# Kernel tuning notes

Measured on AMD Instinct MI355X. Metric: run time of the kernel, lower is better.

The kernel has to match this reference:

```python
import jax, jax.numpy as jnp
import numpy as np

jax.config.update("jax_enable_x64", True)  # original uses torch fp64 for the reciprocal trick

# --- GenericE layout constants ---
N = 32            # NUM_POSITIONS
D = 128           # per-position feature dim
F = N * D         # flattened dim
B = 8192          # batch
NIB_A, NIB_B = 0, 1
SLOT_DIVIDEND, SLOT_DIVISOR, SLOT_REMAINDER, SLOT_QUOTIENT = 2, 3, 4, 5
OP_START, OPCODE, BASE = 64, 3, 2
S = 60.0          # DIV_SCALE
SM_S = 60.0       # SOFTMAX1_SCALE
OP_FLAT = 0 * D + OP_START + OPCODE  # flat index of opcode channel at position 0


def _build_weights():
    # ClearDivSlotsFFN: hidden_dim = 4 slots * 2 units; bake_clear_pair wiring
    cW_up = np.zeros((8, F), np.float32)
    cW_gate = np.zeros((8, F), np.float32)
    cW_down = np.zeros((F, 8), np.float32)
    for i, slot in enumerate([SLOT_DIVIDEND, SLOT_DIVISOR, SLOT_REMAINDER, SLOT_QUOTIENT]):
        h = 2 * i
        # delta[slot] = -(1/S) * relu(S*op_w) * slot_val  -> clears slot when opcode active
        cW_up[h, OP_FLAT] = S
        cW_gate[h, slot] = 1.0
        cW_down[slot, h] = -1.0 / S
        # guard unit of the pair (zero down weight, mirrors gather's guard unit)
        cW_up[h + 1, OP_FLAT] = -S
        cW_gate[h + 1, slot] = -1.0
    # GatherScalarFFN: hidden_dim = N + 1; wiring straight from the source
    H = N + 1
    gW_up = np.zeros((H, F), np.float32)
    gW_gate = np.zeros((H, F), np.float32)
    gW_down = np.zeros((F, H), np.float32)
    dst = 0 * D + SLOT_DIVIDEND
    for i in range(N):
        gW_up[i, OP_FLAT] = S
        gW_gate[i, i * D + NIB_A] = float(BASE ** i)
        gW_down[dst, i] = 1.0 / S
    gW_up[N, OP_FLAT] = -S
    gW_gate[N, dst] = -1.0
    # gW_down[dst, N] = 0.0 (explicit in source)
    return (jnp.asarray(cW_up), jnp.asarray(cW_gate), jnp.asarray(cW_down),
            jnp.asarray(gW_up), jnp.asarray(gW_gate), jnp.asarray(gW_down))


def setup_inputs() -> dict:
    key = jax.random.key(0)
    x = jax.random.uniform(key, (B, N, D), dtype=jnp.float32)
    cW_up, cW_gate, cW_down, gW_up, gW_gate, gW_down = _build_weights()
    base_powers = jnp.asarray([float(BASE ** j) for j in range(N)], dtype=jnp.float64)
    return {"x": x, "cW_up": cW_up, "cW_gate": cW_gate, "cW_down": cW_down,
            "gW_up": gW_up, "gW_gate": gW_gate, "gW_down": gW_down,
            "base_powers": base_powers}


def _ffn_delta(xf, W_up, W_gate, W_down):
    # GenericFlattenedFFN residual delta: W_down @ (relu(W_up x) * (W_gate x))
    h = jax.nn.relu(xf @ W_up.T) * (xf @ W_gate.T)   # [B, H]
    return h @ W_down.T                               # [B, F]


def reference(x, cW_up, cW_gate, cW_down, gW_up, gW_gate, gW_down, base_powers):
    Bc, Nc, Dc = x.shape
    xf = x.reshape(Bc, Nc * Dc)
    # d1 + d2: the two FFN branches (each branch's forward is x + delta, so diff is delta)
    d12 = _ffn_delta(xf, cW_up, cW_gate, cW_down) + _ffn_delta(xf, gW_up, gW_gate, gW_down)
    # d3: Softmax1 reciprocal trick in fp64 (matching torch .double())
    op_w = x[:, 0, OP_START + OPCODE]                         # [B]
    d = x[:, :Nc, NIB_B].astype(jnp.float64)                  # [B, N]
    val = jnp.maximum(d * base_powers, 0.5)
    scores = jnp.where(d > 0.5, jnp.log(val), jnp.float64(-SM_S))
    mx = scores.max(axis=-1, keepdims=True)                   # [B, 1]
    sum_ex = jnp.exp(scores - mx).sum(axis=-1)                # [B]
    recip = jnp.exp(-mx[..., 0]) / jnp.maximum(sum_ex, 1e-30)
    out = x + d12.reshape(Bc, Nc, Dc)
    return out.at[:, 0, SLOT_QUOTIENT].add(op_w * recip.astype(x.dtype))
```

## Files before the change

kernel.cpp:

```cpp
#include <hip/hip_runtime.h>
#include <math.h>


#define FDIM 4096

__global__ __launch_bounds__(256) void div_merged_kernel(
    const float* __restrict__ x, float* __restrict__ out) {
  const long long row = blockIdx.x;
  const float4* __restrict__ x4 = (const float4*)(x + row * (long long)FDIM);
  float4* __restrict__ o4 = (float4*)(out + row * (long long)FDIM);
  const int t = threadIdx.x;

  __shared__ float sa[32];
  __shared__ float sd[32];

  float4 v0 = x4[t];
  float4 v1 = x4[t + 256];
  float4 v2 = x4[t + 512];
  float4 v3 = x4[t + 768];

  if ((t & 31) == 0) {
    const int n0 = t >> 5;
    sa[n0]      = v0.x;  sd[n0]      = v0.y;
    sa[n0 + 8]  = v1.x;  sd[n0 + 8]  = v1.y;
    sa[n0 + 16] = v2.x;  sd[n0 + 16] = v2.y;
    sa[n0 + 24] = v3.x;  sd[n0 + 24] = v3.y;
  }

  if (t >= 2) o4[t] = v0;
  o4[t + 256] = v1;
  o4[t + 512] = v2;
  o4[t + 768] = v3;

  __syncthreads();

  if (t < 32) {
    const float op = __shfl(v0.w, 16);

    const double pw = (double)(1ULL << t);
    const double a  = (double)sa[t];
    const double d  = (double)sd[t];
    double p  = a * pw;
    double ts = (d > 0.5) ? fmax(d * pw, 0.5)
                          : 8.75651076269652e-27;
#pragma unroll
    for (int off = 1; off < 32; off <<= 1) {
      p  += __shfl_xor(p, off);
      ts += __shfl_xor(ts, off);
    }
    const float r60   = fmaxf(60.0f * op, 0.0f);
    const float inv60 = (float)(1.0 / 60.0);
    const float Pf    = (float)p;
    const float recip = (float)(1.0 / ts);

    if (t == 0) {
      const float x2v = v0.z, x3v = v0.w;
      const float dc2 = -((r60 * x2v) * inv60);
      const float dc3 = -((r60 * x3v) * inv60);
      const float dg2 = (r60 * Pf) * inv60;
      v0.z = x2v + (dc2 + dg2);
      v0.w = x3v + dc3;
      o4[0] = v0;
    } else if (t == 1) {
      const float x4v = v0.x, x5v = v0.y;
      const float dc4 = -((r60 * x4v) * inv60);
      const float dc5 = -((r60 * x5v) * inv60);
      v0.x = x4v + dc4;
      v0.y = (x5v + dc5) + op * recip;
      o4[1] = v0;
    }
  }
}

extern "C" void kernel_launch(void* const* d_in, const int* in_sizes, int n_in,
                              void* d_out, int out_size, void* d_ws, size_t ws_size,
                              hipStream_t stream) {
  const float* x = (const float*)d_in[0];
  float* out = (float*)d_out;
  const int rows = in_sizes[0] / FDIM;
  div_merged_kernel<<<rows, 256, 0, stream>>>(x, out);
}
```

Measured before the change: 240.9 us.

## Map one wavefront per row and drop shared memory and block barrier

Each 64-lane wavefront now handles one full row, so a block covers four rows, and each lane holds 16 float4 values. The per-position scalars are reduced in registers with cross-lane shuffles instead of going through shared memory and __syncthreads. Loads are marked nontemporal and all stores are deferred until after the reduction. The aim is to remove barrier stalls and shared-memory traffic in this memory-bound copy, at the cost of more registers per thread and stores that wait for the reduction.

```diff
diff --git a/kernel.cpp b/kernel.cpp
--- a/kernel.cpp
+++ b/kernel.cpp
@@ -3,73 +3,65 @@
 
 
 #define FDIM 4096
+#define ROWS_PER_BLOCK 4
+
+typedef float vf4 __attribute__((ext_vector_type(4)));
 
 __global__ __launch_bounds__(256) void div_merged_kernel(
-    const float* __restrict__ x, float* __restrict__ out) {
-  const long long row = blockIdx.x;
-  const float4* __restrict__ x4 = (const float4*)(x + row * (long long)FDIM);
-  float4* __restrict__ o4 = (float4*)(out + row * (long long)FDIM);
+    const float* __restrict__ x, float* __restrict__ out, int rows) {
   const int t = threadIdx.x;
+  const int wave = t >> 6;
+  const int lane = t & 63;
+  const long long row = (long long)blockIdx.x * ROWS_PER_BLOCK + wave;
+  if (row >= rows) return;
 
-  __shared__ float sa[32];
-  __shared__ float sd[32];
+  const vf4* __restrict__ x4 = (const vf4*)(x + row * (long long)FDIM);
+  vf4* __restrict__ o4 = (vf4*)(out + row * (long long)FDIM);
 
-  float4 v0 = x4[t];
-  float4 v1 = x4[t + 256];
-  float4 v2 = x4[t + 512];
-  float4 v3 = x4[t + 768];
+  vf4 v[16];
+#pragma unroll
+  for (int k = 0; k < 16; ++k)
+    v[k] = __builtin_nontemporal_load(&x4[k * 64 + lane]);
 
-  if ((t & 31) == 0) {
-    const int n0 = t >> 5;
-    sa[n0]      = v0.x;  sd[n0]      = v0.y;
-    sa[n0 + 8]  = v1.x;  sd[n0 + 8]  = v1.y;
-    sa[n0 + 16] = v2.x;  sd[n0 + 16] = v2.y;
-    sa[n0 + 24] = v3.x;  sd[n0 + 24] = v3.y;
+  const double base2 = (lane >= 32) ? 2.0 : 1.0;
+  double p = 0.0, ts = 0.0;
+#pragma unroll
+  for (int k = 0; k < 16; ++k) {
+    const double wk = base2 * (double)(1ULL << (2 * k));
+    p += (double)v[k].x * wk;
+    const double d = (double)v[k].y;
+    ts += (d > 0.5) ? fmax(d * wk, 0.5)
+                    : 8.75651076269652e-27;
+  }
+  p  += __shfl_xor(p, 32);
+  ts += __shfl_xor(ts, 32);
+  p  = __shfl(p, 0);
+  ts = __shfl(ts, 0);
+  const float op = __shfl(v[0].w, 16);
+
+  const float r60   = fmaxf(60.0f * op, 0.0f);
+  const float inv60 = (float)(1.0 / 60.0);
+  const float Pf    = (float)p;
+  const float recip = (float)(1.0 / ts);
+
+  if (lane == 0) {
+    const float x2v = v[0].z, x3v = v[0].w;
+    const float dc2 = -((r60 * x2v) * inv60);
+    const float dc3 = -((r60 * x3v) * inv60);
+    const float dg2 = (r60 * Pf) * inv60;
+    v[0].z = x2v + (dc2 + dg2);
+    v[0].w = x3v + dc3;
+  } else if (lane == 1) {
+    const float x4v = v[0].x, x5v = v[0].y;
+    const float dc4 = -((r60 * x4v) * inv60);
+    const float dc5 = -((r60 * x5v) * inv60);
+    v[0].x = x4v + dc4;
+    v[0].y = (x5v + dc5) + op * recip;
   }
 
-  if (t >= 2) o4[t] = v0;
-  o4[t + 256] = v1;
-  o4[t + 512] = v2;
-  o4[t + 768] = v3;
-
-  __syncthreads();
-
-  if (t < 32) {
-    const float op = __shfl(v0.w, 16);
-
-    const double pw = (double)(1ULL << t);
-    const double a  = (double)sa[t];
-    const double d  = (double)sd[t];
-    double p  = a * pw;
-    double ts = (d > 0.5) ? fmax(d * pw, 0.5)
-                          : 8.75651076269652e-27;
 #pragma unroll
-    for (int off = 1; off < 32; off <<= 1) {
-      p  += __shfl_xor(p, off);
-      ts += __shfl_xor(ts, off);
-    }
-    const float r60   = fmaxf(60.0f * op, 0.0f);
-    const float inv60 = (float)(1.0 / 60.0);
-    const float Pf    = (float)p;
-    const float recip = (float)(1.0 / ts);
-
-    if (t == 0) {
-      const float x2v = v0.z, x3v = v0.w;
-      const float dc2 = -((r60 * x2v) * inv60);
-      const float dc3 = -((r60 * x3v) * inv60);
-      const float dg2 = (r60 * Pf) * inv60;
-      v0.z = x2v + (dc2 + dg2);
-      v0.w = x3v + dc3;
-      o4[0] = v0;
-    } else if (t == 1) {
-      const float x4v = v0.x, x5v = v0.y;
-      const float dc4 = -((r60 * x4v) * inv60);
-      const float dc5 = -((r60 * x5v) * inv60);
-      v0.x = x4v + dc4;
-      v0.y = (x5v + dc5) + op * recip;
-      o4[1] = v0;
-    }
-  }
+  for (int k = 0; k < 16; ++k)
+    o4[k * 64 + lane] = v[k];
 }
 
 extern "C" void kernel_launch(void* const* d_in, const int* in_sizes, int n_in,
@@ -78,5 +70,6 @@
   const float* x = (const float*)d_in[0];
   float* out = (float*)d_out;
   const int rows = in_sizes[0] / FDIM;
-  div_merged_kernel<<<rows, 256, 0, stream>>>(x, out);
+  const int blocks = (rows + ROWS_PER_BLOCK - 1) / ROWS_PER_BLOCK;
+  div_merged_kernel<<<blocks, 256, 0, stream>>>(x, out, rows);
 }
```

After: 236.4 us. No clear change (-1.9%).
